# Performance work log

Hardware: AMD Instinct MI355X
Metric: run time of the kernel (lower is better)

Reference implementation:

```python
import jax, jax.numpy as jnp
import numpy as np

OLD_W, OLD_H = 224, 224   # raster image spatial size (originalShape[2:])
NEW_W, NEW_H = 28, 28     # feature-grid spatial size (newShape[2:])
B, N_SV, HID = 64, 63, 512  # batch, surrounding agents (N-1), LSTM encoder hidden
POS_SCALE = 250.0         # some positions exceed OLD_W to exercise validity masks


def setup_inputs() -> dict:
    key = jax.random.key(0)
    k1, k2, k3 = jax.random.split(key, 3)
    svPositionsAtT0 = jax.random.uniform(k1, (B, N_SV, 3), dtype=jnp.float32) * POS_SCALE
    svEncoding = jax.random.normal(k2, (B, N_SV, HID), dtype=jnp.float32)
    lengths = jax.random.randint(k3, (B,), 0, N_SV, dtype=jnp.int32)
    return {"svPositionsAtT0": svPositionsAtT0, "svEncoding": svEncoding, "lengths": lengths}


def reference(svPositionsAtT0, svEncoding, lengths):
    # Faithful vectorized form of rawToRasterScaleSocialState:
    # sequential per-agent max-writes into a zero-initialized grid == scatter-max.
    b_, n_, hid = svEncoding.shape
    x = svPositionsAtT0[..., 0]                     # (B, N)
    y = svPositionsAtT0[..., 1]
    xIdx = (x * NEW_W / OLD_W).astype(jnp.int32)    # trunc toward zero, as .long()
    yIdx = (y * NEW_H / OLD_H).astype(jnp.int32)
    agent_ids = jnp.arange(n_, dtype=lengths.dtype)[None, :]
    mask = (lengths[:, None] > agent_ids) & (xIdx < NEW_W) & (yIdx < NEW_H)  # (B, N)
    # Invalid agents: write 0 (no-op since grid init is 0 and writes are max-with-0)
    enc = jnp.where(mask[..., None], svEncoding, 0.0)          # (B, N, HID)
    xI = jnp.clip(xIdx, 0, NEW_W - 1)
    yI = jnp.clip(yIdx, 0, NEW_H - 1)
    bI = jnp.broadcast_to(jnp.arange(b_)[:, None], (b_, n_))
    grid = jnp.zeros((b_, hid, NEW_W, NEW_H), dtype=svEncoding.dtype)
    grid = grid.at[bI.ravel(), :, xI.ravel(), yI.ravel()].max(enc.reshape(b_ * n_, hid))
    return grid
```

## Files before the change

kernel.cpp:

```cpp
#include <hip/hip_runtime.h>

#define NSV    63
#define HID    512
#define GW     28
#define GH     28
#define CELLS  (GW * GH)
#define HCHUNK 16
#define NTHREADS 256
#define NQUADS (CELLS / 4)
#define EPAD   20

__device__ __forceinline__ int swz(int u) { return u ^ (((u >> 4) & 3) << 2); }

__global__ __launch_bounds__(NTHREADS)
void scatter_grid_kernel(const float* __restrict__ pos,
                         const float* __restrict__ enc,
                         const int*   __restrict__ lengths,
                         float*       __restrict__ out) {
    const int b      = blockIdx.y;
    const int h_base = blockIdx.x * HCHUNK;
    const int t      = threadIdx.x;

    __shared__ unsigned long long mask_s[CELLS];
    __shared__ float enc_s[NSV * EPAD + 4];

    for (int c = t; c < CELLS; c += NTHREADS) mask_s[c] = 0ull;

    {
        const int n = t >> 2;
        const int q = t & 3;
        if (n < NSV) {
            const float4 v = ((const float4*)(enc + ((size_t)b * NSV + n) * HID + h_base))[q];
            *(float4*)(enc_s + n * EPAD + q * 4) = v;
        }
    }
    __syncthreads();

    if (t < NSV) {
        const float x = pos[((size_t)b * NSV + t) * 3 + 0];
        const float y = pos[((size_t)b * NSV + t) * 3 + 1];
        const int len = lengths[b];
        const int xi = (int)(x * 28.0f / 224.0f);
        const int yi = (int)(y * 28.0f / 224.0f);
        if ((t < len) && (xi < GW) && (yi < GH)) {
            const int xc = min(max(xi, 0), GW - 1);
            const int yc = min(max(yi, 0), GH - 1);
            atomicOr(&mask_s[swz(xc * GH + yc)], 1ull << t);
        }
    }
    __syncthreads();

    if (t < NQUADS) {
        unsigned long long m0, m1, m2, m3;
        {
            const int base = swz(4 * t);
            const ulonglong2 a = *(const ulonglong2*)(mask_s + base);
            const ulonglong2 c = *(const ulonglong2*)(mask_s + base + 2);
            m0 = a.x; m1 = a.y; m2 = c.x; m3 = c.y;
        }

        float4* d4 = (float4*)(out + ((size_t)b * HID + h_base) * CELLS);

        #pragma unroll
        for (int hq = 0; hq < 4; ++hq) {
            float4 v0 = make_float4(0.f, 0.f, 0.f, 0.f);
            float4 v1 = v0, v2 = v0, v3 = v0;
            #pragma unroll
            for (int j = 0; j < 4; ++j) {
                unsigned long long mm = (j == 0) ? m0 : (j == 1) ? m1 : (j == 2) ? m2 : m3;
                while (mm) {
                    const int n = __ffsll(mm) - 1;
                    mm &= mm - 1;
                    const float4 e = *(const float4*)(enc_s + n * EPAD + hq * 4);
                    (&v0.x)[j] = fmaxf((&v0.x)[j], e.x);
                    (&v1.x)[j] = fmaxf((&v1.x)[j], e.y);
                    (&v2.x)[j] = fmaxf((&v2.x)[j], e.z);
                    (&v3.x)[j] = fmaxf((&v3.x)[j], e.w);
                }
            }
            d4[(hq * 4 + 0) * NQUADS + t] = v0;
            d4[(hq * 4 + 1) * NQUADS + t] = v1;
            d4[(hq * 4 + 2) * NQUADS + t] = v2;
            d4[(hq * 4 + 3) * NQUADS + t] = v3;
        }
    }
}

extern "C" void kernel_launch(void* const* d_in, const int* in_sizes, int n_in,
                              void* d_out, int out_size, void* d_ws, size_t ws_size,
                              hipStream_t stream) {
    const float* pos     = (const float*)d_in[0];
    const float* enc     = (const float*)d_in[1];
    const int*   lengths = (const int*)d_in[2];
    float*       out     = (float*)d_out;

    const int B = in_sizes[2];

    dim3 grid(HID / HCHUNK, B);
    dim3 block(NTHREADS);
    scatter_grid_kernel<<<grid, block, 0, stream>>>(pos, enc, lengths, out);
}
```

Measured before the change: 115.4 us.

## Double hidden chunk per block and add all-empty quad fast path

Each block now covers 32 hidden channels instead of 16, which halves the grid and loads the encoding tile in a strided loop. The inner loop now walks one channel at a time with scalar shared-memory reads, replacing the float4-per-4-channels scheme. A fast path writes zeros directly when all four cells of a quad are empty, skipping the bitmask walk. The trade-off is more bitmask iterations per channel in non-empty quads, and half as many blocks are available to hide store latency.

```diff
diff --git a/kernel.cpp b/kernel.cpp
--- a/kernel.cpp
+++ b/kernel.cpp
@@ -5,10 +5,10 @@
 #define GW     28
 #define GH     28
 #define CELLS  (GW * GH)
-#define HCHUNK 16
+#define HCHUNK 32
 #define NTHREADS 256
 #define NQUADS (CELLS / 4)
-#define EPAD   20
+#define EPAD   36
 
 __device__ __forceinline__ int swz(int u) { return u ^ (((u >> 4) & 3) << 2); }
 
@@ -22,19 +22,17 @@
     const int t      = threadIdx.x;
 
     __shared__ unsigned long long mask_s[CELLS];
-    __shared__ float enc_s[NSV * EPAD + 4];
+    __shared__ float enc_s[NSV * EPAD];
 
     for (int c = t; c < CELLS; c += NTHREADS) mask_s[c] = 0ull;
+    __syncthreads();
 
-    {
-        const int n = t >> 2;
-        const int q = t & 3;
-        if (n < NSV) {
-            const float4 v = ((const float4*)(enc + ((size_t)b * NSV + n) * HID + h_base))[q];
-            *(float4*)(enc_s + n * EPAD + q * 4) = v;
-        }
+    for (int i = t; i < NSV * (HCHUNK / 4); i += NTHREADS) {
+        const int n = i >> 3;
+        const int q = i & 7;
+        const float4 v = ((const float4*)(enc + ((size_t)b * NSV + n) * HID + h_base))[q];
+        *(float4*)(enc_s + n * EPAD + q * 4) = v;
     }
-    __syncthreads();
 
     if (t < NSV) {
         const float x = pos[((size_t)b * NSV + t) * 3 + 0];
@@ -61,27 +59,26 @@
 
         float4* d4 = (float4*)(out + ((size_t)b * HID + h_base) * CELLS);
 
-        #pragma unroll
-        for (int hq = 0; hq < 4; ++hq) {
-            float4 v0 = make_float4(0.f, 0.f, 0.f, 0.f);
-            float4 v1 = v0, v2 = v0, v3 = v0;
+        if ((m0 | m1 | m2 | m3) == 0ull) {
+            const float4 z = make_float4(0.f, 0.f, 0.f, 0.f);
             #pragma unroll
-            for (int j = 0; j < 4; ++j) {
-                unsigned long long mm = (j == 0) ? m0 : (j == 1) ? m1 : (j == 2) ? m2 : m3;
-                while (mm) {
-                    const int n = __ffsll(mm) - 1;
-                    mm &= mm - 1;
-                    const float4 e = *(const float4*)(enc_s + n * EPAD + hq * 4);
-                    (&v0.x)[j] = fmaxf((&v0.x)[j], e.x);
-                    (&v1.x)[j] = fmaxf((&v1.x)[j], e.y);
-                    (&v2.x)[j] = fmaxf((&v2.x)[j], e.z);
-                    (&v3.x)[j] = fmaxf((&v3.x)[j], e.w);
+            for (int h = 0; h < HCHUNK; ++h)
+                d4[h * NQUADS + t] = z;
+        } else {
+            for (int h = 0; h < HCHUNK; ++h) {
+                float4 v = make_float4(0.f, 0.f, 0.f, 0.f);
+                #pragma unroll
+                for (int j = 0; j < 4; ++j) {
+                    unsigned long long mm = (j == 0) ? m0 : (j == 1) ? m1
+                                          : (j == 2) ? m2 : m3;
+                    while (mm) {
+                        const int n = __ffsll(mm) - 1;
+                        mm &= mm - 1;
+                        (&v.x)[j] = fmaxf((&v.x)[j], enc_s[n * EPAD + h]);
+                    }
                 }
+                d4[h * NQUADS + t] = v;
             }
-            d4[(hq * 4 + 0) * NQUADS + t] = v0;
-            d4[(hq * 4 + 1) * NQUADS + t] = v1;
-            d4[(hq * 4 + 2) * NQUADS + t] = v2;
-            d4[(hq * 4 + 3) * NQUADS + t] = v3;
         }
     }
 }
```

New measurement: 137.1 us. 1.19x slower.
